# Optimization experiments

Hardware: AMD Instinct MI355X
Metric: run time of the kernel (lower is better)

Reference implementation:

```python
import jax, jax.numpy as jnp
import numpy as np

B, T, E, H = 32768, 11, 128, 20  # batch, STEP_NUM, elem_num, HIDDEN_NUM


def setup_inputs() -> dict:
    key = jax.random.key(0)
    ks = jax.random.split(key, 8)
    u = lambda k, shape, lim: jax.random.uniform(k, shape, jnp.float32, -lim, lim)
    bx = jax.random.normal(ks[0], (B, T, E), jnp.float32)
    by = jax.random.normal(ks[1], (B, E), jnp.float32)
    return dict(
        bx=bx, by=by,
        l=jnp.array([0.9], jnp.float32),
        e=jnp.array([0.5], jnp.float32),
        w1=u(ks[2], (E, 50), np.sqrt(0.02)), b1=jnp.zeros((1, 50), jnp.float32),
        w2=u(ks[3], (50, 100), np.sqrt(0.01)), b2=jnp.zeros((1, 100), jnp.float32),
        w3=u(ks[4], (H, 100), np.sqrt(0.01)), b3=jnp.zeros((1, 100), jnp.float32),
        w4=u(ks[5], (100, E), np.sqrt(1.0 / E)), b4=jnp.zeros((1, E), jnp.float32),
        w=0.05 * jnp.eye(H, dtype=jnp.float32),
        c=u(ks[6], (100, H), np.sqrt(float(H))),
        g=jnp.ones((1, H), jnp.float32),
        b=jnp.ones((1, H), jnp.float32),
    )


def reference(bx, by, l, e, w1, b1, w2, b2, w3, b3, w4, b4, w, c, g, b):
    Bn, Hn = bx.shape[0], w.shape[0]
    # Input MLP is independent per step -> precompute for all steps at once.
    s1 = jax.nn.relu(jnp.einsum('bte,ef->btf', bx, w1) + b1)   # [B,T,50]
    z = jax.nn.relu(jnp.einsum('btf,fg->btg', s1, w2) + b2)    # [B,T,100]
    zc = jnp.einsum('btg,gh->bth', z, c)                       # [B,T,H]

    a0 = jnp.zeros((Bn, Hn, Hn), jnp.float32)  # fast-weight memory
    h0 = jnp.zeros((Bn, Hn), jnp.float32)

    def step(carry, zc_t):
        a, h = carry
        h = jax.nn.relu(h @ w + zc_t)
        # fast-weight outer-product update with decay: a = l*a + e * h h^T
        a = l[0] * a + e[0] * jnp.einsum('bi,bj->bij', h, h)
        # one attractor iteration (inner loop runs once in the source)
        hs = h @ w + zc_t + jnp.einsum('bi,bij->bj', h, a)
        mu = jnp.mean(hs, axis=0, keepdims=True)               # norm over BATCH dim (as in source)
        sig = jnp.sqrt(jnp.mean((hs - mu) ** 2, axis=0, keepdims=True))
        hs = jax.nn.relu(g * (hs - mu) / sig + b)
        return (a, hs), None

    (a, h), _ = jax.lax.scan(step, (a0, h0), jnp.swapaxes(zc, 0, 1))
    h = jax.nn.relu(h @ w3 + b3)
    logits = h @ w4 + b4
    loss = jnp.mean(jnp.sum(-by * jax.nn.log_softmax(logits, axis=-1), axis=-1))
    acc = jnp.mean((jnp.argmax(logits, axis=1) == jnp.argmax(by, axis=1)).astype(jnp.float32))
    return (loss, acc)
```

## Files before the change

### kernel.cpp

```cpp
#include <hip/hip_runtime.h>
#include <hip/hip_bf16.h>

#define BATCH 32768
#define TT 11
#define EE 128
#define HH 20

typedef unsigned short ushort_t;
typedef __attribute__((ext_vector_type(8))) short short8;
typedef __attribute__((ext_vector_type(4))) float f32x4;

#define ZC_OFF   8192
#define HIST_OFF (8192 + 28835840)
#define HS_OFF   (8192 + 2*28835840)
#define W1A_OFF  (HS_OFF + 2621440)
#define W2A_OFF  (W1A_OFF + 32768)
#define CA_OFF   (W2A_OFF + 28672)
#define B1F_OFF  (CA_OFF + 16384)
#define B2F_OFF  (B1F_OFF + 16384)

__device__ __forceinline__ float waveRed(float v) {
    #pragma unroll
    for (int m = 32; m > 0; m >>= 1) v += __shfl_xor(v, m, 64);
    return v;
}

__device__ __forceinline__ void split2(float v, ushort_t& a, ushort_t& b) {
    __hip_bfloat16 h1 = __float2bfloat16(v);
    float r1 = v - __bfloat162float(h1);
    __hip_bfloat16 h2 = __float2bfloat16(r1);
    a = *(ushort_t*)&h1; b = *(ushort_t*)&h2;
}

__device__ __forceinline__ f32x4 mfma16(short8 a, short8 b, f32x4 c) {
    return __builtin_amdgcn_mfma_f32_16x16x32_bf16(a, b, c, 0, 0, 0);
}

union FragU { uint4 v; unsigned int u[4]; short8 s; };

__global__ __launch_bounds__(256) void setup_kernel(
    const float* __restrict__ w1, const float* __restrict__ b1,
    const float* __restrict__ w2, const float* __restrict__ b2,
    const float* __restrict__ c,
    unsigned int* __restrict__ W1A, unsigned int* __restrict__ W2A, unsigned int* __restrict__ CA,
    float* __restrict__ b1f, float* __restrict__ b2f, double* __restrict__ slots)
{
    const int gid = blockIdx.x * 256 + threadIdx.x;
    const int nth = gridDim.x * 256;
    for (int i = gid; i < 1024; i += nth) slots[i] = 0.0;

    for (int i = gid; i < 4096; i += nth) {
        const int r = i & 3, lane = (i >> 2) & 63, nt = (i >> 8) & 3, kt = i >> 10;
        const int m = nt * 16 + (lane & 15);
        const int g = lane >> 4;
        int j0 = 2 * r, j1 = 2 * r + 1;
        int k0 = kt * 32 + ((j0 >= 4) ? 16 : 0) + 4 * g + (j0 & 3);
        int k1 = kt * 32 + ((j1 >= 4) ? 16 : 0) + 4 * g + (j1 & 3);
        float v0 = (m < 50) ? w1[k0 * 50 + m] : 0.f;
        float v1 = (m < 50) ? w1[k1 * 50 + m] : 0.f;
        ushort_t a0, a1, c0, c1;
        split2(v0, a0, a1); split2(v1, c0, c1);
        W1A[(((kt * 4 + nt) * 2 + 0) * 64 + lane) * 4 + r] = a0 | ((unsigned)c0 << 16);
        W1A[(((kt * 4 + nt) * 2 + 1) * 64 + lane) * 4 + r] = a1 | ((unsigned)c1 << 16);
    }
    for (int i = gid; i < 3584; i += nth) {
        const int r = i & 3, lane = (i >> 2) & 63, rest = i >> 8;
        const int nt = rest % 7, kt = rest / 7;
        const int m = nt * 16 + (lane & 15);
        const int g = lane >> 4;
        int j0 = 2 * r, j1 = 2 * r + 1;
        int k0 = kt * 32 + ((j0 >= 4) ? 16 : 0) + 4 * g + (j0 & 3);
        int k1 = kt * 32 + ((j1 >= 4) ? 16 : 0) + 4 * g + (j1 & 3);
        float v0 = (m < 100 && k0 < 50) ? w2[k0 * 100 + m] : 0.f;
        float v1 = (m < 100 && k1 < 50) ? w2[k1 * 100 + m] : 0.f;
        ushort_t a0, a1, c0, c1;
        split2(v0, a0, a1); split2(v1, c0, c1);
        W2A[(((kt * 7 + nt) * 2 + 0) * 64 + lane) * 4 + r] = a0 | ((unsigned)c0 << 16);
        W2A[(((kt * 7 + nt) * 2 + 1) * 64 + lane) * 4 + r] = a1 | ((unsigned)c1 << 16);
    }
    for (int i = gid; i < 2048; i += nth) {
        const int r = i & 3, lane = (i >> 2) & 63, rest = i >> 8;
        const int nt = rest & 1, kt = rest >> 1;
        const int m = nt * 16 + (lane & 15);
        const int g = lane >> 4;
        int j0 = 2 * r, j1 = 2 * r + 1;
        int k0 = kt * 32 + ((j0 >= 4) ? 16 : 0) + 4 * g + (j0 & 3);
        int k1 = kt * 32 + ((j1 >= 4) ? 16 : 0) + 4 * g + (j1 & 3);
        float v0 = (m < 20 && k0 < 100) ? c[k0 * 20 + m] : 0.f;
        float v1 = (m < 20 && k1 < 100) ? c[k1 * 20 + m] : 0.f;
        ushort_t a0, a1, c0, c1;
        split2(v0, a0, a1); split2(v1, c0, c1);
        CA[(((kt * 2 + nt) * 2 + 0) * 64 + lane) * 4 + r] = a0 | ((unsigned)c0 << 16);
        CA[(((kt * 2 + nt) * 2 + 1) * 64 + lane) * 4 + r] = a1 | ((unsigned)c1 << 16);
    }
    for (int i = gid; i < 1024; i += nth) {
        const int r = i & 3, lane = (i >> 2) & 63, nt = i >> 8;
        const int n = nt * 16 + 4 * (lane >> 4) + r;
        b1f[i] = (n < 50) ? b1[n] : 0.f;
    }
    for (int i = gid; i < 1792; i += nth) {
        const int r = i & 3, lane = (i >> 2) & 63, nt = i >> 8;
        const int n = nt * 16 + 4 * (lane >> 4) + r;
        b2f[i] = (n < 100) ? b2[n] : 0.f;
    }
}

__global__ __launch_bounds__(256, 4) void mlp_mfma(
    const float* __restrict__ bx,
    const unsigned int* __restrict__ W1A, const unsigned int* __restrict__ W2A,
    const unsigned int* __restrict__ CA,
    const float* __restrict__ b1f, const float* __restrict__ b2f,
    float* __restrict__ zc)
{
    __shared__ ushort_t Xs[4][2][2048];
    const int tid = threadIdx.x;
    const int lane = tid & 63, wv = tid >> 6;
    const int R = (blockIdx.x * 4 + wv) * 16;
    const int t = R >> 15;
    const int bbase = R & (BATCH - 1);

    {
        const int row = lane >> 2, cg = lane & 3;
        const float4* xp = (const float4*)(bx + ((size_t)(bbase + row) * TT + t) * EE + cg * 32);
        uint2* x0 = (uint2*)Xs[wv][0];
        uint2* x1 = (uint2*)Xs[wv][1];
        #pragma unroll
        for (int q = 0; q < 8; ++q) {
            const float4 v = xp[q];
            const int idx = row * 32 + ((cg * 8 + q) ^ row);
            ushort_t h0[2], h1[2], h2[2], h3[2];
            split2(v.x, h0[0], h0[1]);
            split2(v.y, h1[0], h1[1]);
            split2(v.z, h2[0], h2[1]);
            split2(v.w, h3[0], h3[1]);
            x0[idx] = make_uint2(h0[0] | ((unsigned)h1[0] << 16), h2[0] | ((unsigned)h3[0] << 16));
            x1[idx] = make_uint2(h0[1] | ((unsigned)h1[1] << 16), h2[1] | ((unsigned)h3[1] << 16));
        }
    }

    const int rrow = lane & 15, g = lane >> 4;
    const uint4* W1A4 = (const uint4*)W1A;
    const uint4* W2A4 = (const uint4*)W2A;
    const uint4* CA4  = (const uint4*)CA;
    const float4* b1f4 = (const float4*)b1f;
    const float4* b2f4 = (const float4*)b2f;

    f32x4 D1[4];
    #pragma unroll
    for (int nt = 0; nt < 4; ++nt) D1[nt] = (f32x4){0.f, 0.f, 0.f, 0.f};
    #pragma unroll
    for (int kt = 0; kt < 4; ++kt) {
        FragU B[2];
        #pragma unroll
        for (int sp = 0; sp < 2; ++sp) {
            const uint2* xs = (const uint2*)Xs[wv][sp];
            const int kb = kt * 8 + g;
            uint2 lo = xs[rrow * 32 + (kb ^ rrow)];
            uint2 hi = xs[rrow * 32 + ((kb + 4) ^ rrow)];
            B[sp].u[0] = lo.x; B[sp].u[1] = lo.y; B[sp].u[2] = hi.x; B[sp].u[3] = hi.y;
        }
        #pragma unroll
        for (int nt = 0; nt < 4; ++nt) {
            FragU A0, A1;
            A0.v = W1A4[((kt * 4 + nt) * 2 + 0) * 64 + lane];
            A1.v = W1A4[((kt * 4 + nt) * 2 + 1) * 64 + lane];
            D1[nt] = mfma16(A1.s, B[0].s, D1[nt]);
            D1[nt] = mfma16(A0.s, B[1].s, D1[nt]);
            D1[nt] = mfma16(A0.s, B[0].s, D1[nt]);
        }
    }

    f32x4 D2[7];
    #pragma unroll
    for (int nt = 0; nt < 7; ++nt) D2[nt] = (f32x4){0.f, 0.f, 0.f, 0.f};
    #pragma unroll
    for (int kt2 = 0; kt2 < 2; ++kt2) {
        FragU B[2];
        #pragma unroll
        for (int half = 0; half < 2; ++half) {
            const int nt = 2 * kt2 + half;
            const float4 bv = b1f4[nt * 64 + lane];
            #pragma unroll
            for (int rp = 0; rp < 2; ++rp) {
                float v0 = fmaxf(D1[nt][2 * rp]     + bv[2 * rp],     0.f);
                float v1 = fmaxf(D1[nt][2 * rp + 1] + bv[2 * rp + 1], 0.f);
                ushort_t s00, s01, s10, s11;
                split2(v0, s00, s01); split2(v1, s10, s11);
                B[0].u[half * 2 + rp] = s00 | ((unsigned)s10 << 16);
                B[1].u[half * 2 + rp] = s01 | ((unsigned)s11 << 16);
            }
        }
        #pragma unroll
        for (int nt2 = 0; nt2 < 7; ++nt2) {
            FragU A0, A1;
            A0.v = W2A4[((kt2 * 7 + nt2) * 2 + 0) * 64 + lane];
            A1.v = W2A4[((kt2 * 7 + nt2) * 2 + 1) * 64 + lane];
            D2[nt2] = mfma16(A1.s, B[0].s, D2[nt2]);
            D2[nt2] = mfma16(A0.s, B[1].s, D2[nt2]);
            D2[nt2] = mfma16(A0.s, B[0].s, D2[nt2]);
        }
    }

    f32x4 D3[2];
    D3[0] = (f32x4){0.f, 0.f, 0.f, 0.f};
    D3[1] = (f32x4){0.f, 0.f, 0.f, 0.f};
    #pragma unroll
    for (int kt3 = 0; kt3 < 4; ++kt3) {
        FragU B[2];
        #pragma unroll
        for (int half = 0; half < 2; ++half) {
            const int nt = 2 * kt3 + half;
            if (nt < 7) {
                const float4 bv = b2f4[nt * 64 + lane];
                #pragma unroll
                for (int rp = 0; rp < 2; ++rp) {
                    float v0 = fmaxf(D2[nt][2 * rp]     + bv[2 * rp],     0.f);
                    float v1 = fmaxf(D2[nt][2 * rp + 1] + bv[2 * rp + 1], 0.f);
                    ushort_t s00, s01, s10, s11;
                    split2(v0, s00, s01); split2(v1, s10, s11);
                    B[0].u[half * 2 + rp] = s00 | ((unsigned)s10 << 16);
                    B[1].u[half * 2 + rp] = s01 | ((unsigned)s11 << 16);
                }
            } else {
                B[0].u[2] = B[0].u[3] = 0u;
                B[1].u[2] = B[1].u[3] = 0u;
            }
        }
        #pragma unroll
        for (int nt3 = 0; nt3 < 2; ++nt3) {
            FragU A0, A1;
            A0.v = CA4[((kt3 * 2 + nt3) * 2 + 0) * 64 + lane];
            A1.v = CA4[((kt3 * 2 + nt3) * 2 + 1) * 64 + lane];
            D3[nt3] = mfma16(A1.s, B[0].s, D3[nt3]);
            D3[nt3] = mfma16(A0.s, B[1].s, D3[nt3]);
            D3[nt3] = mfma16(A0.s, B[0].s, D3[nt3]);
        }
    }

    const int bcol = bbase + rrow;
    #pragma unroll
    for (int r = 0; r < 4; ++r) {
        const int h = 4 * g + r;
        zc[((size_t)(t * HH + h) << 15) + bcol] = D3[0][r];
    }
    if (g == 0) {
        #pragma unroll
        for (int r = 0; r < 4; ++r) {
            zc[((size_t)(t * HH + 16 + r) << 15) + bcol] = D3[1][r];
        }
    }
}

__global__ __launch_bounds__(256) void step_kernel(
    const float* __restrict__ zc, const float* __restrict__ lp, const float* __restrict__ ep,
    const float* __restrict__ w, const float* __restrict__ g, const float* __restrict__ bb,
    float* __restrict__ hist, float* __restrict__ hs_buf, double* __restrict__ slots, int t)
{
    __shared__ float red[4][40];
    const int tid = threadIdx.x;
    const int p = tid & 1;
    const int sb = tid >> 1;
    const int b = blockIdx.x * 128 + sb;
    const int lane = tid & 63, wv = tid >> 6;
    const int jb = 10 * p;
    const float l0 = lp[0], e0 = ep[0];

    float h[10];
    if (t == 0) {
        #pragma unroll
        for (int jj = 0; jj < 10; ++jj) h[jj] = 0.f;
    } else {
        #pragma unroll
        for (int jj = 0; jj < 10; ++jj) {
            const int j = jb + jj;
            const double s1 = slots[(t - 1) * 64 + j];
            const double s2 = slots[(t - 1) * 64 + HH + j];
            const double mu = s1 * (1.0 / 32768.0);
            const double var = s2 * (1.0 / 32768.0) - mu * mu;
            const float muf = (float)mu;
            const float rsig = 1.0f / sqrtf((float)var);
            const float hv = hs_buf[(j << 15) + b];
            h[jj] = fmaxf(fmaf(g[j] * rsig, hv - muf, bb[j]), 0.f);
        }
    }

    float zct[10];
    #pragma unroll
    for (int jj = 0; jj < 10; ++jj) zct[jj] = zc[((t * HH + jb + jj) << 15) + b];

    float hn[10];
    {
        float po[20];
        #pragma unroll
        for (int j = 0; j < 20; ++j) {
            float a = 0.f;
            #pragma unroll
            for (int ii = 0; ii < 10; ++ii) a = fmaf(h[ii], w[(jb + ii) * HH + j], a);
            po[j] = a;
        }
        #pragma unroll
        for (int jj = 0; jj < 10; ++jj) {
            const float mine = p ? po[10 + jj] : po[jj];
            const float send = p ? po[jj] : po[10 + jj];
            const float recv = __shfl_xor(send, 1, 64);
            hn[jj] = fmaxf(mine + recv + zct[jj], 0.f);
        }
    }
    #pragma unroll
    for (int jj = 0; jj < 10; ++jj) hist[((t * HH + jb + jj) << 15) + b] = hn[jj];

    float pv[10];
    {
        float dp = 0.f;
        #pragma unroll
        for (int jj = 0; jj < 10; ++jj) dp = fmaf(hn[jj], hn[jj], dp);
        const float d = dp + __shfl_xor(dp, 1, 64);
        const float cd = e0 * d;
        #pragma unroll
        for (int jj = 0; jj < 10; ++jj) pv[jj] = cd * hn[jj];
    }
    float coef = e0 * l0;
    #pragma unroll 1
    for (int s = t - 1; s >= 0; --s) {
        float tv[10];
        #pragma unroll
        for (int jj = 0; jj < 10; ++jj) tv[jj] = hist[((s * HH + jb + jj) << 15) + b];
        float dp = 0.f;
        #pragma unroll
        for (int jj = 0; jj < 10; ++jj) dp = fmaf(hn[jj], tv[jj], dp);
        const float d = dp + __shfl_xor(dp, 1, 64);
        const float cd = coef * d;
        #pragma unroll
        for (int jj = 0; jj < 10; ++jj) pv[jj] = fmaf(cd, tv[jj], pv[jj]);
        coef *= l0;
    }

    float hs[10];
    {
        float po[20];
        #pragma unroll
        for (int j = 0; j < 20; ++j) {
            float a = 0.f;
            #pragma unroll
            for (int ii = 0; ii < 10; ++ii) a = fmaf(hn[ii], w[(jb + ii) * HH + j], a);
            po[j] = a;
        }
        #pragma unroll
        for (int jj = 0; jj < 10; ++jj) {
            const float mine = p ? po[10 + jj] : po[jj];
            const float send = p ? po[jj] : po[10 + jj];
            const float recv = __shfl_xor(send, 1, 64);
            hs[jj] = mine + recv + zct[jj] + pv[jj];
            hs_buf[((jb + jj) << 15) + b] = hs[jj];
        }
    }

    float sm[10], sq[10];
    #pragma unroll
    for (int jj = 0; jj < 10; ++jj) { sm[jj] = hs[jj]; sq[jj] = hs[jj] * hs[jj]; }
    #pragma unroll
    for (int m = 2; m <= 32; m <<= 1) {
        #pragma unroll
        for (int jj = 0; jj < 10; ++jj) {
            sm[jj] += __shfl_xor(sm[jj], m, 64);
            sq[jj] += __shfl_xor(sq[jj], m, 64);
        }
    }
    if (lane < 2) {
        #pragma unroll
        for (int jj = 0; jj < 10; ++jj) {
            red[wv][jb + jj] = sm[jj];
            red[wv][20 + jb + jj] = sq[jj];
        }
    }
    __syncthreads();
    if (tid < 40) {
        atomicAdd(&slots[t * 64 + tid],
                  (double)(red[0][tid] + red[1][tid] + red[2][tid] + red[3][tid]));
    }
}

__global__ __launch_bounds__(256, 2) void head_kernel(
    const float* __restrict__ hs_buf, const float* __restrict__ by,
    const float* __restrict__ g, const float* __restrict__ bb,
    const float* __restrict__ w3, const float* __restrict__ b3,
    const float* __restrict__ w4, const float* __restrict__ b4,
    double* __restrict__ slots)
{
    __shared__ float hfs[100][64];
    __shared__ float cpm[4][64], cps[4][64], cdot[4][64], csby[4][64], cbym[4][64];
    __shared__ int   cidx[4][64], cbyidx[4][64];
    const int tid = threadIdx.x;
    const int lane = tid & 63;
    const int p = tid >> 6;
    const int b = blockIdx.x * 64 + lane;

    float h[HH];
    #pragma unroll
    for (int j = 0; j < HH; ++j) {
        const double s1 = slots[10 * 64 + j];
        const double s2 = slots[10 * 64 + HH + j];
        const double mu = s1 * (1.0 / 32768.0);
        const double var = s2 * (1.0 / 32768.0) - mu * mu;
        const float muf = (float)mu;
        const float rsig = 1.0f / sqrtf((float)var);
        const float hv = hs_buf[(j << 15) + b];
        h[j] = fmaxf(fmaf(g[j] * rsig, hv - muf, bb[j]), 0.f);
    }

    #pragma unroll
    for (int k = 0; k < 25; ++k) {
        const int f = p * 25 + k;
        float a = b3[f];
        #pragma unroll
        for (int i = 0; i < HH; ++i) a = fmaf(h[i], w3[i * 100 + f], a);
        hfs[f][lane] = fmaxf(a, 0.f);
    }
    __syncthreads();

    float lg[32];
    {
        const float* b4c = b4 + p * 32;
        #pragma unroll
        for (int u = 0; u < 32; ++u) lg[u] = b4c[u];
    }
    for (int k = 0; k < 100; ++k) {
        const float hv = hfs[k][lane];
        const float* wr = w4 + k * EE + p * 32;
        #pragma unroll
        for (int u = 0; u < 32; ++u) lg[u] = fmaf(hv, wr[u], lg[u]);
    }

    float pm = lg[0]; int pidx = 0;
    #pragma unroll
    for (int u = 1; u < 32; ++u) { if (lg[u] > pm) { pm = lg[u]; pidx = u; } }
    float ps = 0.f;
    #pragma unroll
    for (int u = 0; u < 32; ++u) ps += expf(lg[u] - pm);

    const float* byp = by + (size_t)b * EE + p * 32;
    float dotp = 0.f, sbyp = 0.f, bym = -3.402823e38f; int byi = 0;
    #pragma unroll
    for (int u4 = 0; u4 < 8; ++u4) {
        const float4 v = *(const float4*)(byp + u4 * 4);
        const int u = u4 * 4;
        if (v.x > bym) { bym = v.x; byi = u; }
        if (v.y > bym) { bym = v.y; byi = u + 1; }
        if (v.z > bym) { bym = v.z; byi = u + 2; }
        if (v.w > bym) { bym = v.w; byi = u + 3; }
        dotp = fmaf(v.x, lg[u], dotp);
        dotp = fmaf(v.y, lg[u + 1], dotp);
        dotp = fmaf(v.z, lg[u + 2], dotp);
        dotp = fmaf(v.w, lg[u + 3], dotp);
        sbyp += v.x + v.y + v.z + v.w;
    }

    cpm[p][lane] = pm;  cps[p][lane] = ps;  cdot[p][lane] = dotp;  csby[p][lane] = sbyp;
    cidx[p][lane] = p * 32 + pidx;
    cbym[p][lane] = bym; cbyidx[p][lane] = p * 32 + byi;
    __syncthreads();

    if (p == 0) {
        float gm = cpm[0][lane];
        #pragma unroll
        for (int q = 1; q < 4; ++q) gm = fmaxf(gm, cpm[q][lane]);
        float se = 0.f, dot = 0.f, sby = 0.f;
        #pragma unroll
        for (int q = 0; q < 4; ++q) {
            se  += cps[q][lane] * expf(cpm[q][lane] - gm);
            dot += cdot[q][lane];
            sby += csby[q][lane];
        }
        float cm = cpm[0][lane]; int am = cidx[0][lane];
        #pragma unroll
        for (int q = 1; q < 4; ++q) { if (cpm[q][lane] > cm) { cm = cpm[q][lane]; am = cidx[q][lane]; } }
        float bm = cbym[0][lane]; int byam = cbyidx[0][lane];
        #pragma unroll
        for (int q = 1; q < 4; ++q) { if (cbym[q][lane] > bm) { bm = cbym[q][lane]; byam = cbyidx[q][lane]; } }

        const float loss_i = -dot + (gm + logf(se)) * sby;
        const float acc_i = (am == byam) ? 1.f : 0.f;
        const float ls = waveRed(loss_i);
        const float as = waveRed(acc_i);
        if (lane == 0) {
            atomicAdd(&slots[704], (double)ls);
            atomicAdd(&slots[705], (double)as);
        }
    }
}

__global__ void finalize_kernel(const double* __restrict__ slots, float* __restrict__ out) {
    out[0] = (float)(slots[704] * (1.0 / 32768.0));
    out[1] = (float)(slots[705] * (1.0 / 32768.0));
}

extern "C" void kernel_launch(void* const* d_in, const int* in_sizes, int n_in,
                              void* d_out, int out_size, void* d_ws, size_t ws_size,
                              hipStream_t stream) {
    const float* bx = (const float*)d_in[0];
    const float* by = (const float*)d_in[1];
    const float* l  = (const float*)d_in[2];
    const float* e  = (const float*)d_in[3];
    const float* w1 = (const float*)d_in[4];
    const float* b1 = (const float*)d_in[5];
    const float* w2 = (const float*)d_in[6];
    const float* b2 = (const float*)d_in[7];
    const float* w3 = (const float*)d_in[8];
    const float* b3 = (const float*)d_in[9];
    const float* w4 = (const float*)d_in[10];
    const float* b4 = (const float*)d_in[11];
    const float* w  = (const float*)d_in[12];
    const float* c  = (const float*)d_in[13];
    const float* g  = (const float*)d_in[14];
    const float* bb = (const float*)d_in[15];

    double* slots = (double*)d_ws;
    float*  zcw   = (float*)((char*)d_ws + ZC_OFF);
    float*  hist  = (float*)((char*)d_ws + HIST_OFF);
    float*  hs    = (float*)((char*)d_ws + HS_OFF);
    unsigned int* W1A = (unsigned int*)((char*)d_ws + W1A_OFF);
    unsigned int* W2A = (unsigned int*)((char*)d_ws + W2A_OFF);
    unsigned int* CA  = (unsigned int*)((char*)d_ws + CA_OFF);
    float* b1f = (float*)((char*)d_ws + B1F_OFF);
    float* b2f = (float*)((char*)d_ws + B2F_OFF);
    float*  outp  = (float*)d_out;

    hipLaunchKernelGGL(setup_kernel, dim3(16), dim3(256), 0, stream,
                       w1, b1, w2, b2, c, W1A, W2A, CA, b1f, b2f, slots);
    hipLaunchKernelGGL(mlp_mfma, dim3(5632), dim3(256), 0, stream,
                       bx, W1A, W2A, CA, b1f, b2f, zcw);
    for (int t = 0; t < TT; ++t) {
        hipLaunchKernelGGL(step_kernel, dim3(256), dim3(256), 0, stream,
                           zcw, l, e, w, g, bb, hist, hs, slots, t);
    }
    hipLaunchKernelGGL(head_kernel, dim3(512), dim3(256), 0, stream,
                       hs, by, g, bb, w3, b3, w4, b4, slots);
    hipLaunchKernelGGL(finalize_kernel, dim3(1), dim3(1), 0, stream, slots, outp);
}
```

Baseline: 335.7 us.

## Double MLP rows per wave, drop LDS staging, template step kernel on timestep

The MLP kernel now has each wave process 32 batch rows instead of 16. It loads input fragments straight from global memory into registers rather than staging them through LDS, and it reuses each weight fragment load across two MFMA chains. The step kernel is templated on the timestep, so the history loop fully unrolls and all history, zc and previous hs loads are issued up front to overlap their latency. The cost is higher register pressure in both kernels and fewer MLP blocks, with the occupancy hint removed from the MLP launch bounds.

Result: slower. 433.1 us (+29.0%).

```diff
diff --git a/kernel.cpp b/kernel.cpp
--- a/kernel.cpp
+++ b/kernel.cpp
@@ -105,125 +105,128 @@
     }
 }
 
-__global__ __launch_bounds__(256, 4) void mlp_mfma(
+__device__ __forceinline__ void buildB(const float4 lo, const float4 hi, FragU& B0, FragU& B1) {
+    ushort_t a[8], b[8];
+    split2(lo.x, a[0], b[0]); split2(lo.y, a[1], b[1]);
+    split2(lo.z, a[2], b[2]); split2(lo.w, a[3], b[3]);
+    split2(hi.x, a[4], b[4]); split2(hi.y, a[5], b[5]);
+    split2(hi.z, a[6], b[6]); split2(hi.w, a[7], b[7]);
+    #pragma unroll
+    for (int r = 0; r < 4; ++r) {
+        B0.u[r] = a[2 * r] | ((unsigned)a[2 * r + 1] << 16);
+        B1.u[r] = b[2 * r] | ((unsigned)b[2 * r + 1] << 16);
+    }
+}
+
+__device__ __forceinline__ void actSplit(const f32x4 D, const float4 bv, int half, FragU* B) {
+    #pragma unroll
+    for (int rp = 0; rp < 2; ++rp) {
+        float v0 = fmaxf(D[2 * rp]     + bv[2 * rp],     0.f);
+        float v1 = fmaxf(D[2 * rp + 1] + bv[2 * rp + 1], 0.f);
+        ushort_t s00, s01, s10, s11;
+        split2(v0, s00, s01); split2(v1, s10, s11);
+        B[0].u[half * 2 + rp] = s00 | ((unsigned)s10 << 16);
+        B[1].u[half * 2 + rp] = s01 | ((unsigned)s11 << 16);
+    }
+}
+
+__global__ __launch_bounds__(256) void mlp_mfma(
     const float* __restrict__ bx,
     const unsigned int* __restrict__ W1A, const unsigned int* __restrict__ W2A,
     const unsigned int* __restrict__ CA,
     const float* __restrict__ b1f, const float* __restrict__ b2f,
     float* __restrict__ zc)
 {
-    __shared__ ushort_t Xs[4][2][2048];
     const int tid = threadIdx.x;
     const int lane = tid & 63, wv = tid >> 6;
-    const int R = (blockIdx.x * 4 + wv) * 16;
+    const int R = (blockIdx.x * 4 + wv) * 32;
     const int t = R >> 15;
     const int bbase = R & (BATCH - 1);
-
-    {
-        const int row = lane >> 2, cg = lane & 3;
-        const float4* xp = (const float4*)(bx + ((size_t)(bbase + row) * TT + t) * EE + cg * 32);
-        uint2* x0 = (uint2*)Xs[wv][0];
-        uint2* x1 = (uint2*)Xs[wv][1];
-        #pragma unroll
-        for (int q = 0; q < 8; ++q) {
-            const float4 v = xp[q];
-            const int idx = row * 32 + ((cg * 8 + q) ^ row);
-            ushort_t h0[2], h1[2], h2[2], h3[2];
-            split2(v.x, h0[0], h0[1]);
-            split2(v.y, h1[0], h1[1]);
-            split2(v.z, h2[0], h2[1]);
-            split2(v.w, h3[0], h3[1]);
-            x0[idx] = make_uint2(h0[0] | ((unsigned)h1[0] << 16), h2[0] | ((unsigned)h3[0] << 16));
-            x1[idx] = make_uint2(h0[1] | ((unsigned)h1[1] << 16), h2[1] | ((unsigned)h3[1] << 16));
-        }
-    }
-
-    const int rrow = lane & 15, g = lane >> 4;
+    const int srow = lane & 15, g = lane >> 4;
+
+    const float* xp0 = bx + ((size_t)(bbase + srow) * TT + t) * EE;
+    const float* xp1 = bx + ((size_t)(bbase + 16 + srow) * TT + t) * EE;
+
+    float4 xl0[4], xh0[4], xl1[4], xh1[4];
+    #pragma unroll
+    for (int kt = 0; kt < 4; ++kt) {
+        xl0[kt] = *(const float4*)(xp0 + kt * 32 + 4 * g);
+        xh0[kt] = *(const float4*)(xp0 + kt * 32 + 16 + 4 * g);
+        xl1[kt] = *(const float4*)(xp1 + kt * 32 + 4 * g);
+        xh1[kt] = *(const float4*)(xp1 + kt * 32 + 16 + 4 * g);
+    }
+
     const uint4* W1A4 = (const uint4*)W1A;
     const uint4* W2A4 = (const uint4*)W2A;
     const uint4* CA4  = (const uint4*)CA;
     const float4* b1f4 = (const float4*)b1f;
     const float4* b2f4 = (const float4*)b2f;
 
-    f32x4 D1[4];
-    #pragma unroll
-    for (int nt = 0; nt < 4; ++nt) D1[nt] = (f32x4){0.f, 0.f, 0.f, 0.f};
+    f32x4 D1a[4], D1b[4];
+    #pragma unroll
+    for (int nt = 0; nt < 4; ++nt) { D1a[nt] = (f32x4){0,0,0,0}; D1b[nt] = (f32x4){0,0,0,0}; }
     #pragma unroll
     for (int kt = 0; kt < 4; ++kt) {
-        FragU B[2];
-        #pragma unroll
-        for (int sp = 0; sp < 2; ++sp) {
-            const uint2* xs = (const uint2*)Xs[wv][sp];
-            const int kb = kt * 8 + g;
-            uint2 lo = xs[rrow * 32 + (kb ^ rrow)];
-            uint2 hi = xs[rrow * 32 + ((kb + 4) ^ rrow)];
-            B[sp].u[0] = lo.x; B[sp].u[1] = lo.y; B[sp].u[2] = hi.x; B[sp].u[3] = hi.y;
-        }
+        FragU Ba[2], Bb[2];
+        buildB(xl0[kt], xh0[kt], Ba[0], Ba[1]);
+        buildB(xl1[kt], xh1[kt], Bb[0], Bb[1]);
         #pragma unroll
         for (int nt = 0; nt < 4; ++nt) {
             FragU A0, A1;
             A0.v = W1A4[((kt * 4 + nt) * 2 + 0) * 64 + lane];
             A1.v = W1A4[((kt * 4 + nt) * 2 + 1) * 64 + lane];
-            D1[nt] = mfma16(A1.s, B[0].s, D1[nt]);
-            D1[nt] = mfma16(A0.s, B[1].s, D1[nt]);
-            D1[nt] = mfma16(A0.s, B[0].s, D1[nt]);
-        }
-    }
-
-    f32x4 D2[7];
-    #pragma unroll
-    for (int nt = 0; nt < 7; ++nt) D2[nt] = (f32x4){0.f, 0.f, 0.f, 0.f};
+            D1a[nt] = mfma16(A1.s, Ba[0].s, D1a[nt]);
+            D1a[nt] = mfma16(A0.s, Ba[1].s, D1a[nt]);
+            D1a[nt] = mfma16(A0.s, Ba[0].s, D1a[nt]);
+            D1b[nt] = mfma16(A1.s, Bb[0].s, D1b[nt]);
+            D1b[nt] = mfma16(A0.s, Bb[1].s, D1b[nt]);
+            D1b[nt] = mfma16(A0.s, Bb[0].s, D1b[nt]);
+        }
+    }
+
+    f32x4 D2a[7], D2b[7];
+    #pragma unroll
+    for (int nt = 0; nt < 7; ++nt) { D2a[nt] = (f32x4){0,0,0,0}; D2b[nt] = (f32x4){0,0,0,0}; }
     #pragma unroll
     for (int kt2 = 0; kt2 < 2; ++kt2) {
-        FragU B[2];
+        FragU Ba[2], Bb[2];
         #pragma unroll
         for (int half = 0; half < 2; ++half) {
             const int nt = 2 * kt2 + half;
             const float4 bv = b1f4[nt * 64 + lane];
-            #pragma unroll
-            for (int rp = 0; rp < 2; ++rp) {
-                float v0 = fmaxf(D1[nt][2 * rp]     + bv[2 * rp],     0.f);
-                float v1 = fmaxf(D1[nt][2 * rp + 1] + bv[2 * rp + 1], 0.f);
-                ushort_t s00, s01, s10, s11;
-                split2(v0, s00, s01); split2(v1, s10, s11);
-                B[0].u[half * 2 + rp] = s00 | ((unsigned)s10 << 16);
-                B[1].u[half * 2 + rp] = s01 | ((unsigned)s11 << 16);
-            }
+            actSplit(D1a[nt], bv, half, Ba);
+            actSplit(D1b[nt], bv, half, Bb);
         }
         #pragma unroll
         for (int nt2 = 0; nt2 < 7; ++nt2) {
             FragU A0, A1;
             A0.v = W2A4[((kt2 * 7 + nt2) * 2 + 0) * 64 + lane];
             A1.v = W2A4[((kt2 * 7 + nt2) * 2 + 1) * 64 + lane];
-            D2[nt2] = mfma16(A1.s, B[0].s, D2[nt2]);
-            D2[nt2] = mfma16(A0.s, B[1].s, D2[nt2]);
-            D2[nt2] = mfma16(A0.s, B[0].s, D2[nt2]);
-        }
-    }
-
-    f32x4 D3[2];
-    D3[0] = (f32x4){0.f, 0.f, 0.f, 0.f};
-    D3[1] = (f32x4){0.f, 0.f, 0.f, 0.f};
+            D2a[nt2] = mfma16(A1.s, Ba[0].s, D2a[nt2]);
+            D2a[nt2] = mfma16(A0.s, Ba[1].s, D2a[nt2]);
+            D2a[nt2] = mfma16(A0.s, Ba[0].s, D2a[nt2]);
+            D2b[nt2] = mfma16(A1.s, Bb[0].s, D2b[nt2]);
+            D2b[nt2] = mfma16(A0.s, Bb[1].s, D2b[nt2]);
+            D2b[nt2] = mfma16(A0.s, Bb[0].s, D2b[nt2]);
+        }
+    }
+
+    f32x4 D3a[2], D3b[2];
+    D3a[0] = (f32x4){0,0,0,0}; D3a[1] = (f32x4){0,0,0,0};
+    D3b[0] = (f32x4){0,0,0,0}; D3b[1] = (f32x4){0,0,0,0};
     #pragma unroll
     for (int kt3 = 0; kt3 < 4; ++kt3) {
-        FragU B[2];
+        FragU Ba[2], Bb[2];
         #pragma unroll
         for (int half = 0; half < 2; ++half) {
             const int nt = 2 * kt3 + half;
             if (nt < 7) {
                 const float4 bv = b2f4[nt * 64 + lane];
-                #pragma unroll
-                for (int rp = 0; rp < 2; ++rp) {
-                    float v0 = fmaxf(D2[nt][2 * rp]     + bv[2 * rp],     0.f);
-                    float v1 = fmaxf(D2[nt][2 * rp + 1] + bv[2 * rp + 1], 0.f);
-                    ushort_t s00, s01, s10, s11;
-                    split2(v0, s00, s01); split2(v1, s10, s11);
-                    B[0].u[half * 2 + rp] = s00 | ((unsigned)s10 << 16);
-                    B[1].u[half * 2 + rp] = s01 | ((unsigned)s11 << 16);
-                }
+                actSplit(D2a[nt], bv, half, Ba);
+                actSplit(D2b[nt], bv, half, Bb);
             } else {
-                B[0].u[2] = B[0].u[3] = 0u;
-                B[1].u[2] = B[1].u[3] = 0u;
+                Ba[0].u[2] = Ba[0].u[3] = 0u; Ba[1].u[2] = Ba[1].u[3] = 0u;
+                Bb[0].u[2] = Bb[0].u[3] = 0u; Bb[1].u[2] = Bb[1].u[3] = 0u;
             }
         }
         #pragma unroll
@@ -231,30 +234,36 @@
             FragU A0, A1;
             A0.v = CA4[((kt3 * 2 + nt3) * 2 + 0) * 64 + lane];
             A1.v = CA4[((kt3 * 2 + nt3) * 2 + 1) * 64 + lane];
-            D3[nt3] = mfma16(A1.s, B[0].s, D3[nt3]);
-            D3[nt3] = mfma16(A0.s, B[1].s, D3[nt3]);
-            D3[nt3] = mfma16(A0.s, B[0].s, D3[nt3]);
-        }
-    }
-
-    const int bcol = bbase + rrow;
+            D3a[nt3] = mfma16(A1.s, Ba[0].s, D3a[nt3]);
+            D3a[nt3] = mfma16(A0.s, Ba[1].s, D3a[nt3]);
+            D3a[nt3] = mfma16(A0.s, Ba[0].s, D3a[nt3]);
+            D3b[nt3] = mfma16(A1.s, Bb[0].s, D3b[nt3]);
+            D3b[nt3] = mfma16(A0.s, Bb[1].s, D3b[nt3]);
+            D3b[nt3] = mfma16(A0.s, Bb[0].s, D3b[nt3]);
+        }
+    }
+
+    const int bcol0 = bbase + srow, bcol1 = bbase + 16 + srow;
     #pragma unroll
     for (int r = 0; r < 4; ++r) {
         const int h = 4 * g + r;
-        zc[((size_t)(t * HH + h) << 15) + bcol] = D3[0][r];
+        zc[((size_t)(t * HH + h) << 15) + bcol0] = D3a[0][r];
+        zc[((size_t)(t * HH + h) << 15) + bcol1] = D3b[0][r];
     }
     if (g == 0) {
         #pragma unroll
         for (int r = 0; r < 4; ++r) {
-            zc[((size_t)(t * HH + 16 + r) << 15) + bcol] = D3[1][r];
-        }
-    }
-}
-
+            zc[((size_t)(t * HH + 16 + r) << 15) + bcol0] = D3a[1][r];
+            zc[((size_t)(t * HH + 16 + r) << 15) + bcol1] = D3b[1][r];
+        }
+    }
+}
+
+template<int TC>
 __global__ __launch_bounds__(256) void step_kernel(
     const float* __restrict__ zc, const float* __restrict__ lp, const float* __restrict__ ep,
     const float* __restrict__ w, const float* __restrict__ g, const float* __restrict__ bb,
-    float* __restrict__ hist, float* __restrict__ hs_buf, double* __restrict__ slots, int t)
+    float* __restrict__ hist, float* __restrict__ hs_buf, double* __restrict__ slots)
 {
     __shared__ float red[4][40];
     const int tid = threadIdx.x;
@@ -265,28 +274,39 @@
     const int jb = 10 * p;
     const float l0 = lp[0], e0 = ep[0];
 
+    float tv[TC > 0 ? TC : 1][10];
+    #pragma unroll
+    for (int s = 0; s < TC; ++s) {
+        #pragma unroll
+        for (int jj = 0; jj < 10; ++jj)
+            tv[s][jj] = hist[((s * HH + jb + jj) << 15) + b];
+    }
+    float zct[10];
+    #pragma unroll
+    for (int jj = 0; jj < 10; ++jj) zct[jj] = zc[((TC * HH + jb + jj) << 15) + b];
+    float hprev[10];
+    if (TC > 0) {
+        #pragma unroll
+        for (int jj = 0; jj < 10; ++jj) hprev[jj] = hs_buf[((jb + jj) << 15) + b];
+    }
+
     float h[10];
-    if (t == 0) {
+    if (TC == 0) {
         #pragma unroll
         for (int jj = 0; jj < 10; ++jj) h[jj] = 0.f;
     } else {
         #pragma unroll
         for (int jj = 0; jj < 10; ++jj) {
             const int j = jb + jj;
-            const double s1 = slots[(t - 1) * 64 + j];
-            const double s2 = slots[(t - 1) * 64 + HH + j];
+            const double s1 = slots[(TC - 1) * 64 + j];
+            const double s2 = slots[(TC - 1) * 64 + HH + j];
             const double mu = s1 * (1.0 / 32768.0);
             const double var = s2 * (1.0 / 32768.0) - mu * mu;
             const float muf = (float)mu;
             const float rsig = 1.0f / sqrtf((float)var);
-            const float hv = hs_buf[(j << 15) + b];
-            h[jj] = fmaxf(fmaf(g[j] * rsig, hv - muf, bb[j]), 0.f);
-        }
-    }
-
-    float zct[10];
-    #pragma unroll
-    for (int jj = 0; jj < 10; ++jj) zct[jj] = zc[((t * HH + jb + jj) << 15) + b];
+            h[jj] = fmaxf(fmaf(g[j] * rsig, hprev[jj] - muf, bb[j]), 0.f);
+        }
+    }
 
     float hn[10];
     {
@@ -307,7 +327,7 @@
         }
     }
     #pragma unroll
-    for (int jj = 0; jj < 10; ++jj) hist[((t * HH + jb + jj) << 15) + b] = hn[jj];
+    for (int jj = 0; jj < 10; ++jj) hist[((TC * HH + jb + jj) << 15) + b] = hn[jj];
 
     float pv[10];
     {
@@ -319,20 +339,20 @@
         #pragma unroll
         for (int jj = 0; jj < 10; ++jj) pv[jj] = cd * hn[jj];
     }
-    float coef = e0 * l0;
-    #pragma unroll 1
-    for (int s = t - 1; s >= 0; --s) {
-        float tv[10];
-        #pragma unroll
-        for (int jj = 0; jj < 10; ++jj) tv[jj] = hist[((s * HH + jb + jj) << 15) + b];
-        float dp = 0.f;
-        #pragma unroll
-        for (int jj = 0; jj < 10; ++jj) dp = fmaf(hn[jj], tv[jj], dp);
-        const float d = dp + __shfl_xor(dp, 1, 64);
-        const float cd = coef * d;
-        #pragma unroll
-        for (int jj = 0; jj < 10; ++jj) pv[jj] = fmaf(cd, tv[jj], pv[jj]);
-        coef *= l0;
+    if (TC > 0) {
+        float coef = e0 * l0;
+        #pragma unroll
+        for (int si = 0; si < TC; ++si) {
+            const int s = TC - 1 - si;
+            float dp = 0.f;
+            #pragma unroll
+            for (int jj = 0; jj < 10; ++jj) dp = fmaf(hn[jj], tv[s][jj], dp);
+            const float d = dp + __shfl_xor(dp, 1, 64);
+            const float cd = coef * d;
+            #pragma unroll
+            for (int jj = 0; jj < 10; ++jj) pv[jj] = fmaf(cd, tv[s][jj], pv[jj]);
+            coef *= l0;
+        }
     }
 
     float hs[10];
@@ -375,7 +395,7 @@
     }
     __syncthreads();
     if (tid < 40) {
-        atomicAdd(&slots[t * 64 + tid],
+        atomicAdd(&slots[TC * 64 + tid],
                   (double)(red[0][tid] + red[1][tid] + red[2][tid] + red[3][tid]));
     }
 }
@@ -527,12 +547,13 @@
 
     hipLaunchKernelGGL(setup_kernel, dim3(16), dim3(256), 0, stream,
                        w1, b1, w2, b2, c, W1A, W2A, CA, b1f, b2f, slots);
-    hipLaunchKernelGGL(mlp_mfma, dim3(5632), dim3(256), 0, stream,
+    hipLaunchKernelGGL(mlp_mfma, dim3(2816), dim3(256), 0, stream,
                        bx, W1A, W2A, CA, b1f, b2f, zcw);
-    for (int t = 0; t < TT; ++t) {
-        hipLaunchKernelGGL(step_kernel, dim3(256), dim3(256), 0, stream,
-                           zcw, l, e, w, g, bb, hist, hs, slots, t);
-    }
+#define LSTEP(T) hipLaunchKernelGGL((step_kernel<T>), dim3(256), dim3(256), 0, stream, \
+                                    zcw, l, e, w, g, bb, hist, hs, slots)
+    LSTEP(0); LSTEP(1); LSTEP(2); LSTEP(3); LSTEP(4); LSTEP(5);
+    LSTEP(6); LSTEP(7); LSTEP(8); LSTEP(9); LSTEP(10);
+#undef LSTEP
     hipLaunchKernelGGL(head_kernel, dim3(512), dim3(256), 0, stream,
                        hs, by, g, bb, w3, b3, w4, b4, slots);
     hipLaunchKernelGGL(finalize_kernel, dim3(1), dim3(1), 0, stream, slots, outp);
```
